# Kernel tuning notes

Hardware: AMD Instinct MI355X
Metric: run time of the kernel (lower is better)

Reference implementation:

```python
import jax, jax.numpy as jnp
import numpy as np

DIM = 1024
NUM_HEADS = 16
HEAD_DIM = DIM // NUM_HEADS


def apply_rotary_embed(x, thetas):
    # x: (..., seq, d), thetas: (seq, d) broadcast over leading dims
    x1, x2 = jnp.split(x, 2, axis=-1)
    x_rot = jnp.concatenate([-x2, x1], axis=-1)
    return x * jnp.cos(thetas) + x_rot * jnp.sin(thetas)


def setup_inputs() -> dict:
    key = jax.random.key(0)
    ks = jax.random.split(key, 8)
    B, Nx, Nc = 4, 1024, 2048
    x = jax.random.normal(ks[0], (B, Nx, DIM), dtype=jnp.float32)
    c = jax.random.normal(ks[1], (B, Nc, DIM), dtype=jnp.float32)
    x_pos_embed = jax.random.normal(ks[2], (Nx, HEAD_DIM), dtype=jnp.float32)
    c_pos_embed = jax.random.normal(ks[3], (Nc, HEAD_DIM), dtype=jnp.float32)
    s = 1.0 / np.sqrt(DIM)
    Wq = jax.random.normal(ks[4], (DIM, DIM), dtype=jnp.float32) * s
    Wkv = jax.random.normal(ks[5], (DIM, 2 * DIM), dtype=jnp.float32) * s
    Wproj = jax.random.normal(ks[6], (DIM, DIM), dtype=jnp.float32) * s
    bproj = jnp.zeros((DIM,), dtype=jnp.float32)
    return {"x": x, "c": c, "x_pos_embed": x_pos_embed, "c_pos_embed": c_pos_embed,
            "Wq": Wq, "Wkv": Wkv, "Wproj": Wproj, "bproj": bproj}


def reference(x, c, x_pos_embed, c_pos_embed, Wq, Wkv, Wproj, bproj):
    B, Nx, D = x.shape
    Nc = c.shape[1]
    H, hd = NUM_HEADS, HEAD_DIM
    # Q projection -> (B, H, Nx, hd)
    q = (x @ Wq).reshape(B, Nx, H, hd).transpose(0, 2, 1, 3)
    q = apply_rotary_embed(q, x_pos_embed)
    # KV projection -> k, v each (B, H, Nc, hd)
    kv = (c @ Wkv).reshape(B, Nc, 2, H, hd).transpose(2, 0, 3, 1, 4)
    k, v = kv[0], kv[1]
    k = apply_rotary_embed(k, c_pos_embed)
    # scaled dot-product attention (dropout p=0 -> identity)
    scale = 1.0 / np.sqrt(hd).astype(np.float32)
    attn = jnp.einsum('bhqd,bhkd->bhqk', q, k) * scale
    attn = jax.nn.softmax(attn, axis=-1)
    out = jnp.einsum('bhqk,bhkd->bhqd', attn, v)
    out = out.transpose(0, 2, 1, 3).reshape(B, Nx, D)
    return out @ Wproj + bproj
```

## Files before the change

### kernel.cpp

```cpp
#include <hip/hip_runtime.h>
#include <math.h>

#define DIMC  1024
#define NHEAD 16
#define HD    64
#define NB    4
#define NX    1024
#define NC    2048
#define KD    1024

typedef _Float16 half_t;
typedef __attribute__((ext_vector_type(8))) _Float16 h8;
typedef __attribute__((ext_vector_type(4))) _Float16 h4;
typedef __attribute__((ext_vector_type(2))) __fp16 fp16x2;
typedef __attribute__((ext_vector_type(4))) float f32x4;

#define QSCALE 0.1803368801111244f
#define NEGM  -8.656170245333781f

__device__ __forceinline__ void gload_lds16(const half_t* g, half_t* l) {
    __builtin_amdgcn_global_load_lds(
        (__attribute__((address_space(1))) void*)(g),
        (__attribute__((address_space(3))) void*)(l), 16, 0, 0);
}

__device__ __forceinline__ void wtile(const float* __restrict__ W,
                                      half_t* __restrict__ Wt, int N, int IMG,
                                      int bx, int by, int t)
{
    __shared__ half_t T[64][72];
    const int k0 = by * 64, n0 = bx * 64;
    const int kr = t >> 2, c0 = (t & 3) << 4;
    const float* src = W + (size_t)(k0 + kr) * N + n0 + c0;
#pragma unroll
    for (int j = 0; j < 16; j += 4) {
        float4 v = *(const float4*)(src + j);
        T[c0 + j + 0][kr] = (half_t)v.x;
        T[c0 + j + 1][kr] = (half_t)v.y;
        T[c0 + j + 2][kr] = (half_t)v.z;
        T[c0 + j + 3][kr] = (half_t)v.w;
    }
    __syncthreads();
    const int nr = t >> 2, kc = (t & 3) << 4;
    if (!IMG) {
        half_t* dst = Wt + (size_t)(n0 + nr) * KD + k0 + kc;
        *(int4*)dst       = *(const int4*)&T[nr][kc];
        *(int4*)(dst + 8) = *(const int4*)&T[nr][kc + 8];
    } else {
        const int n = n0 + nr;
        const int ntile = n >> 8, rr = n & 255;
        const int s0 = kc >> 3;
        half_t* base = Wt + ((size_t)(ntile * 16 + by) * 256 + rr) * 64;
        *(int4*)(base + ((s0 ^ (rr & 7)) << 3))       = *(const int4*)&T[nr][kc];
        *(int4*)(base + (((s0 + 1) ^ (rr & 7)) << 3)) = *(const int4*)&T[nr][kc + 8];
    }
}

__global__ __launch_bounds__(256) void prep(
    const float* __restrict__ x, half_t* __restrict__ xh,
    const float* __restrict__ c, half_t* __restrict__ ch,
    const float* __restrict__ xpe, const float* __restrict__ cpe,
    float* __restrict__ xct, float* __restrict__ xst,
    float* __restrict__ cct, float* __restrict__ cst,
    const float* __restrict__ Wq,  half_t* __restrict__ Wqt,
    const float* __restrict__ Wkv, half_t* __restrict__ Wkt,
    const float* __restrict__ Wp,  half_t* __restrict__ Wpt)
{
    const int bid = blockIdx.x, t = threadIdx.x;
    if (bid < 1024) {
        if (bid < 256)      wtile(Wq,  Wqt, DIMC, 0,     bid & 15,         bid >> 4,         t);
        else if (bid < 768) wtile(Wkv, Wkt, 2 * DIMC, 1, (bid - 256) & 31, (bid - 256) >> 5, t);
        else                wtile(Wp,  Wpt, DIMC, 0,     (bid - 768) & 15, (bid - 768) >> 4, t);
    } else if (bid < 7168) {
        const int nx = NB * NX * DIMC;
        const int i = ((bid - 1024) * 256 + t) * 8;
        const float* s;
        h8 o;
        if (i < nx) {
            s = x + i;
            float4 a = *(const float4*)(s);
            float4 b = *(const float4*)(s + 4);
            o[0] = (half_t)a.x; o[1] = (half_t)a.y; o[2] = (half_t)a.z; o[3] = (half_t)a.w;
            o[4] = (half_t)b.x; o[5] = (half_t)b.y; o[6] = (half_t)b.z; o[7] = (half_t)b.w;
            *(h8*)(xh + i) = o;
        } else {
            const int j = i - nx;
            s = c + j;
            float4 a = *(const float4*)(s);
            float4 b = *(const float4*)(s + 4);
            o[0] = (half_t)a.x; o[1] = (half_t)a.y; o[2] = (half_t)a.z; o[3] = (half_t)a.w;
            o[4] = (half_t)b.x; o[5] = (half_t)b.y; o[6] = (half_t)b.z; o[7] = (half_t)b.w;
            const int R = j >> 10, k = j & 1023;
            const int mt = R >> 8, r = R & 255, kt = k >> 6, sl = (k & 63) >> 3;
            *(h8*)(ch + ((size_t)(mt * 16 + kt) * 256 + r) * 64 + ((sl ^ (r & 7)) << 3)) = o;
        }
    } else {
        const int i = (bid - 7168) * 256 + t;
        if (i < NX * HD) {
            const float th = xpe[i];
            xct[i] = cosf(th); xst[i] = sinf(th);
        } else {
            const int j = i - NX * HD;
            const float th = cpe[j];
            cct[j] = cosf(th); cst[j] = sinf(th);
        }
    }
}

template <int MODE, int BN>
__global__ __launch_bounds__(256) void hgemm(
    const half_t* __restrict__ Ag, const half_t* __restrict__ Bt,
    const float* __restrict__ ct, const float* __restrict__ st,
    const float* __restrict__ bias,
    void* __restrict__ out0, void* __restrict__ out1)
{
    constexpr int MI = (BN == 128) ? 4 : 2;
    constexpr int BLOADS = BN / 32;
    __shared__ half_t As[2][8192];
    __shared__ half_t Bs[2][BN * 64];

    const int tid = threadIdx.x;
    const int w = tid >> 6, lane = tid & 63;
    const int lr = lane & 15, lg = lane >> 4;
    const int wrOff = (BN == 128) ? (w >> 1) * 64 : w * 32;
    const int wcOff = (BN == 128) ? (w & 1) * 64 : 0;

    int lin = (int)blockIdx.x;
    lin = (lin & 7) * ((int)gridDim.x >> 3) + (lin >> 3);
    const int m0 = (lin >> 4) * 128, n0 = (lin & 15) * BN;

    f32x4 acc[MI][4];
#pragma unroll
    for (int i = 0; i < MI; ++i)
#pragma unroll
        for (int j = 0; j < 4; ++j) acc[i][j] = f32x4{0.f, 0.f, 0.f, 0.f};

    size_t gA[4], gB[BLOADS];
    int loff[4];
#pragma unroll
    for (int c = 0; c < 4; ++c) {
        const int L = c * 4096 + w * 1024 + lane * 16;
        const int row = L >> 7;
        const int ss = ((L >> 4) & 7) ^ (row & 7);
        gA[c] = (size_t)(m0 + row) * KD + ss * 8;
        if (c < BLOADS) gB[c] = (size_t)(n0 + row) * KD + ss * 8;
        loff[c] = c * 2048 + w * 512;
    }

#define HSTAGE(buf, kk) do {                                               \
        _Pragma("unroll")                                                  \
        for (int c = 0; c < 4; ++c) {                                      \
            gload_lds16(Ag + gA[c] + (kk) * 64, &As[buf][loff[c]]);        \
            if (c < BLOADS) gload_lds16(Bt + gB[c] + (kk) * 64, &Bs[buf][loff[c]]); \
        }                                                                  \
    } while (0)

    HSTAGE(0, 0);
    asm volatile("s_waitcnt vmcnt(0)" ::: "memory");
    __builtin_amdgcn_s_barrier();
    __builtin_amdgcn_sched_barrier(0);

    for (int k = 0; k < KD / 64; ++k) {
        const int cb = k & 1;
        if (k + 1 < KD / 64) {
            HSTAGE(cb ^ 1, k + 1);
            if constexpr (BLOADS == 4)
                asm volatile("s_waitcnt vmcnt(8)" ::: "memory");
            else
                asm volatile("s_waitcnt vmcnt(6)" ::: "memory");
        } else {
            asm volatile("s_waitcnt vmcnt(0)" ::: "memory");
        }
        __builtin_amdgcn_s_barrier();
        __builtin_amdgcn_sched_barrier(0);

        __builtin_amdgcn_s_setprio(1);
#pragma unroll
        for (int kc = 0; kc < 2; ++kc) {
            h8 af[MI], bf[4];
#pragma unroll
            for (int mi = 0; mi < MI; ++mi) {
                const int r = wrOff + mi * 16 + lr;
                af[mi] = *(const h8*)&As[cb][r * 64 + (((kc * 4 + lg) ^ (r & 7)) << 3)];
            }
#pragma unroll
            for (int ni = 0; ni < 4; ++ni) {
                const int r = wcOff + ni * 16 + lr;
                bf[ni] = *(const h8*)&Bs[cb][r * 64 + (((kc * 4 + lg) ^ (r & 7)) << 3)];
            }
#pragma unroll
            for (int mi = 0; mi < MI; ++mi)
#pragma unroll
                for (int ni = 0; ni < 4; ++ni)
                    acc[mi][ni] = __builtin_amdgcn_mfma_f32_16x16x32_f16(
                        af[mi], bf[ni], acc[mi][ni], 0, 0, 0);
        }
        __builtin_amdgcn_s_setprio(0);

        __builtin_amdgcn_s_barrier();
        __builtin_amdgcn_sched_barrier(0);
    }
#undef HSTAGE

    if (MODE == 2) {
        float* o = (float*)out0;
#pragma unroll
        for (int ni = 0; ni < 4; ++ni) {
            const int col = n0 + ni * 16 + lr;
            const float bv = bias[col];
#pragma unroll
            for (int mi = 0; mi < MI; ++mi)
#pragma unroll
                for (int r = 0; r < 4; ++r) {
                    const int row = m0 + wrOff + mi * 16 + lg * 4 + r;
                    o[(size_t)row * DIMC + col] = acc[mi][ni][r] + bv;
                }
        }
        return;
    }

    if (MODE == 0) {
        half_t* Qw = (half_t*)out0;
        const int h = n0 >> 6;
#pragma unroll
        for (int mi = 0; mi < MI; ++mi)
#pragma unroll
            for (int r = 0; r < 4; ++r) {
                const int row = m0 + wrOff + mi * 16 + lg * 4 + r;
                const int bb = row >> 10, nn = row & (NX - 1);
                const float* cr = ct + nn * HD;
                const float* sr = st + nn * HD;
                half_t* op = Qw + (((size_t)(bb * NHEAD + h)) * NX + nn) * HD;
#pragma unroll
                for (int ni = 0; ni < 4; ++ni) {
                    const int d = ni * 16 + lr;
                    const float val = acc[mi][ni][r];
                    const float pv  = acc[mi][ni ^ 2][r];
                    op[d] = (half_t)((val * cr[d] + (ni < 2 ? -pv : pv) * sr[d]) * QSCALE);
                }
            }
    }
}

__global__ __launch_bounds__(512, 2) void hgemm_kv(
    const half_t* __restrict__ Aimg, const half_t* __restrict__ Bimg,
    const float* __restrict__ ct, const float* __restrict__ st,
    half_t* __restrict__ Kw, half_t* __restrict__ Vw)
{
    __shared__ half_t lds[65536];

    const int tid = threadIdx.x;
    const int w = tid >> 6, lane = tid & 63;
    const int lr = lane & 15, lg = lane >> 4;
    const int wr = w >> 2, wc = w & 3;
    const int wrOff = wr * 128, wcOff = wc * 64;

    int lin = (int)blockIdx.x;
    lin = (lin & 7) * 32 + (lin >> 3);
    const int mt = lin >> 3, nt = lin & 7;
    const int m0 = mt * 256, n0 = nt * 256;

    const half_t* Ablk = Aimg + (size_t)mt * 262144;
    const half_t* Bblk = Bimg + (size_t)nt * 262144;
    const int so2 = w * 512 + lane * 8;

    f32x4 acc[8][4];
#pragma unroll
    for (int i = 0; i < 8; ++i)
#pragma unroll
        for (int j = 0; j < 4; ++j) acc[i][j] = f32x4{0.f, 0.f, 0.f, 0.f};
    h8 af[2][2];
    h8 bf[4][2];

#define ISSUEH(SRC, DSTOFF) do {                                     \
        gload_lds16((SRC) + so2,        &lds[(DSTOFF) + w * 512]);   \
        gload_lds16((SRC) + 4096 + so2, &lds[(DSTOFF) + 4096 + w * 512]); \
    } while (0)

#define PHASE(MI0, AOFF, BOFF, READBF, STG, GATE) do {               \
        _Pragma("unroll")                                            \
        for (int kc = 0; kc < 2; ++kc)                               \
        _Pragma("unroll")                                            \
        for (int d = 0; d < 2; ++d) {                                \
            const int r_ = wrOff + ((MI0) + d) * 16 + lr;            \
            af[d][kc] = *(const h8*)&lds[(AOFF) + r_ * 64 + (((kc * 4 + lg) ^ (r_ & 7)) << 3)]; \
        }                                                            \
        if (READBF) {                                                \
            _Pragma("unroll")                                        \
            for (int ni = 0; ni < 4; ++ni)                           \
            _Pragma("unroll")                                        \
            for (int kc = 0; kc < 2; ++kc) {                         \
                const int rb = wcOff + ni * 16 + lr;                 \
                bf[ni][kc] = *(const h8*)&lds[(BOFF) + rb * 64 + (((kc * 4 + lg) ^ (rb & 7)) << 3)]; \
            }                                                        \
        }                                                            \
        STG;                                                         \
        __builtin_amdgcn_sched_barrier(0);                           \
        __builtin_amdgcn_s_barrier();                                \
        __builtin_amdgcn_s_setprio(1);                               \
        _Pragma("unroll")                                            \
        for (int d = 0; d < 2; ++d)                                  \
        _Pragma("unroll")                                            \
        for (int ni = 0; ni < 4; ++ni)                               \
        _Pragma("unroll")                                            \
        for (int kc = 0; kc < 2; ++kc)                               \
            acc[(MI0) + d][ni] = __builtin_amdgcn_mfma_f32_16x16x32_f16( \
                af[d][kc], bf[ni][kc], acc[(MI0) + d][ni], 0, 0, 0); \
        __builtin_amdgcn_s_setprio(0);                               \
        GATE;                                                        \
        __builtin_amdgcn_s_barrier();                                \
    } while (0)

#define GATE4 asm volatile("s_waitcnt vmcnt(4)" ::: "memory")
#define GATE0 asm volatile("s_waitcnt vmcnt(0)" ::: "memory")
#define NOG   ((void)0)

    ISSUEH(Ablk, 0);          ISSUEH(Ablk + 8192, 8192);
    ISSUEH(Bblk, 32768);      ISSUEH(Bblk + 8192, 32768 + 8192);
    __builtin_amdgcn_sched_barrier(0);
    ISSUEH(Bblk + 16384, 49152); ISSUEH(Bblk + 16384 + 8192, 49152 + 8192);
    asm volatile("s_waitcnt vmcnt(4)" ::: "memory");
    __builtin_amdgcn_s_barrier();

    for (int i = 0; i < 7; ++i) {
        const half_t* An1 = Ablk + (size_t)(2 * i + 1) * 16384;
        const half_t* An2 = Ablk + (size_t)(2 * i + 2) * 16384;
        const half_t* Bn2 = Bblk + (size_t)(2 * i + 2) * 16384;
        const half_t* Bn3 = Bblk + (size_t)(2 * i + 3) * 16384;
        PHASE(0, 0,     32768, true,  ISSUEH(An1, 16384),               NOG);
        PHASE(2, 0,     32768, false, ISSUEH(An1 + 8192, 16384 + 8192), NOG);
        PHASE(4, 0,     32768, false, ISSUEH(Bn2, 32768),               NOG);
        PHASE(6, 0,     32768, false, ISSUEH(Bn2 + 8192, 32768 + 8192), GATE4);
        PHASE(0, 16384, 49152, true,  ISSUEH(An2, 0),                   NOG);
        PHASE(2, 16384, 49152, false, ISSUEH(An2 + 8192, 8192),         NOG);
        PHASE(4, 16384, 49152, false, ISSUEH(Bn3, 49152),               NOG);
        PHASE(6, 16384, 49152, false, ISSUEH(Bn3 + 8192, 49152 + 8192), GATE4);
    }
    {
        const half_t* A15 = Ablk + (size_t)15 * 16384;
        PHASE(0, 0,     32768, true,  ISSUEH(A15, 16384),               NOG);
        PHASE(2, 0,     32768, false, ISSUEH(A15 + 8192, 16384 + 8192), NOG);
        PHASE(4, 0,     32768, false, NOG,                              NOG);
        PHASE(6, 0,     32768, false, NOG,                              GATE0);
        PHASE(0, 16384, 49152, true,  NOG,                              NOG);
        PHASE(2, 16384, 49152, false, NOG,                              NOG);
        PHASE(4, 16384, 49152, false, NOG,                              NOG);
        PHASE(6, 16384, 49152, false, NOG,                              NOG);
    }
#undef PHASE
#undef ISSUEH
#undef GATE4
#undef GATE0
#undef NOG

    const bool isK = (n0 < DIMC);
    const int h = ((n0 & (DIMC - 1)) >> 6) + wc;
#pragma unroll
    for (int mi = 0; mi < 8; ++mi)
#pragma unroll
        for (int r = 0; r < 4; ++r) {
            const int row = m0 + wrOff + mi * 16 + lg * 4 + r;
            const int bb = row >> 11, nn = row & (NC - 1);
            const int tt = nn >> 6, rr = nn & 63;
            const size_t tbase = ((size_t)(bb * NHEAD + h) * 32 + tt) * 4096;
            const float* cr = ct + nn * HD;
            const float* sr = st + nn * HD;
#pragma unroll
            for (int ni = 0; ni < 4; ++ni) {
                const int d = ni * 16 + lr;
                const float val = acc[mi][ni][r];
                if (isK) {
                    const float pv = acc[mi][ni ^ 2][r];
                    Kw[tbase + rr * 64 + ((((d >> 3) ^ (rr & 7)) << 3) | (d & 7))] =
                        (half_t)(val * cr[d] + (ni < 2 ? -pv : pv) * sr[d]);
                } else {
                    Vw[tbase + d * 64 + ((((rr >> 3) ^ (d & 7)) << 3) | (rr & 7))] =
                        (half_t)val;
                }
            }
        }
}

__global__ __launch_bounds__(256) void attn_mfma(
    const half_t* __restrict__ Q, const half_t* __restrict__ Kg,
    const half_t* __restrict__ Vg, half_t* __restrict__ O)
{
    __shared__ half_t Ks[2][4096];
    __shared__ half_t Vs[2][4096];
    __shared__ half_t Ps[8192];

    const int tid = threadIdx.x;
    const int w = tid >> 6, lane = tid & 63;
    const int lr = lane & 15, lg = lane >> 4;
    const int e7 = lr & 7;

    const int sid = (blockIdx.x & 7) * 64 + (blockIdx.x >> 3);
    const int bh = sid >> 3;
    const int q0 = (sid & 7) * 128;
    const int b = bh >> 4, h = bh & 15;

    const half_t* qbase = Q + ((size_t)bh * NX + q0 + w * 16 + lr) * HD + lg * 8;
    const h8 qf0a = *(const h8*)(qbase);
    const h8 qf1a = *(const h8*)(qbase + 32);
    const h8 qf0b = *(const h8*)(qbase + (size_t)64 * HD);
    const h8 qf1b = *(const h8*)(qbase + (size_t)64 * HD + 32);

    f32x4 acc[2][4];
#pragma unroll
    for (int qb = 0; qb < 2; ++qb)
#pragma unroll
        for (int i = 0; i < 4; ++i) acc[qb][i] = f32x4{0.f, 0.f, 0.f, 0.f};
    f32x4 accl[2] = {{0.f, 0.f, 0.f, 0.f}, {0.f, 0.f, 0.f, 0.f}};

    h8 vone;
#pragma unroll
    for (int i = 0; i < 8; ++i) vone[i] = (half_t)(lr == 0 ? 1.0f : 0.0f);

    const half_t* Kt = Kg + (size_t)bh * 32 * 4096;
    const half_t* Vt = Vg + (size_t)bh * 32 * 4096;
    const int so = w * 512 + lane * 8;

#define STAGE(bi, t) do {                                           \
        const half_t* kg_ = Kt + (size_t)(t) * 4096;                \
        const half_t* vg_ = Vt + (size_t)(t) * 4096;                \
        gload_lds16(kg_ + so,        &Ks[bi][w * 512]);             \
        gload_lds16(kg_ + 2048 + so, &Ks[bi][2048 + w * 512]);      \
        gload_lds16(vg_ + so,        &Vs[bi][w * 512]);             \
        gload_lds16(vg_ + 2048 + so, &Vs[bi][2048 + w * 512]);      \
    } while (0)

    STAGE(0, 0);
    asm volatile("s_waitcnt vmcnt(0)" ::: "memory");
    __builtin_amdgcn_s_barrier();
    __builtin_amdgcn_sched_barrier(0);

    const int rowq = w * 16 + lr;

    for (int t = 0; t < NC / 64; ++t) {
        const int cur = t & 1;
        if (t + 1 < NC / 64) {
            STAGE(cur ^ 1, t + 1);
            asm volatile("s_waitcnt vmcnt(8)" ::: "memory");
        } else {
            asm volatile("s_waitcnt vmcnt(0)" ::: "memory");
        }
        __builtin_amdgcn_s_barrier();
        __builtin_amdgcn_sched_barrier(0);

        h8 kfr[4][2];
#pragma unroll
        for (int cb = 0; cb < 4; ++cb) {
            const int r = cb * 16 + lr;
            kfr[cb][0] = *(const h8*)&Ks[cur][r * 64 + ((lg ^ e7) << 3)];
            kfr[cb][1] = *(const h8*)&Ks[cur][r * 64 + (((4 + lg) ^ e7) << 3)];
        }

#pragma unroll
        for (int qb = 0; qb < 2; ++qb) {
            const h8 q0f = qb ? qf0b : qf0a;
            const h8 q1f = qb ? qf1b : qf1a;
            const int rowp = qb * 64 + rowq;

            f32x4 sc[4];
            __builtin_amdgcn_s_setprio(1);
#pragma unroll
            for (int cb = 0; cb < 4; ++cb) {
                f32x4 a = {NEGM, NEGM, NEGM, NEGM};
                a = __builtin_amdgcn_mfma_f32_16x16x32_f16(kfr[cb][0], q0f, a, 0, 0, 0);
                a = __builtin_amdgcn_mfma_f32_16x16x32_f16(kfr[cb][1], q1f, a, 0, 0, 0);
                sc[cb] = a;
            }
            __builtin_amdgcn_s_setprio(0);

#pragma unroll
            for (int cb = 0; cb < 4; ++cb) {
                fp16x2 a01 = __builtin_amdgcn_cvt_pkrtz(exp2f(sc[cb][0]), exp2f(sc[cb][1]));
                fp16x2 a23 = __builtin_amdgcn_cvt_pkrtz(exp2f(sc[cb][2]), exp2f(sc[cb][3]));
                union { h4 h; uint2 u; } pw;
                pw.u.x = *(unsigned int*)&a01;
                pw.u.y = *(unsigned int*)&a23;
                const int s = cb * 2 + (lg >> 1);
                *(h4*)&Ps[rowp * 64 + ((s ^ e7) << 3) + (lg & 1) * 4] = pw.h;
            }
        }

        h8 pf[2][2];
#pragma unroll
        for (int qb = 0; qb < 2; ++qb) {
            const int rowp = qb * 64 + rowq;
            pf[qb][0] = *(const h8*)&Ps[rowp * 64 + ((lg ^ e7) << 3)];
            pf[qb][1] = *(const h8*)&Ps[rowp * 64 + (((4 + lg) ^ e7) << 3)];
        }

        __builtin_amdgcn_s_setprio(1);
#pragma unroll
        for (int db = 0; db < 4; ++db) {
            const int rd = db * 16 + lr;
            const h8 vf0 = *(const h8*)&Vs[cur][rd * 64 + ((lg ^ e7) << 3)];
            const h8 vf1 = *(const h8*)&Vs[cur][rd * 64 + (((4 + lg) ^ e7) << 3)];
#pragma unroll
            for (int qb = 0; qb < 2; ++qb) {
                acc[qb][db] = __builtin_amdgcn_mfma_f32_16x16x32_f16(pf[qb][0], vf0, acc[qb][db], 0, 0, 0);
                acc[qb][db] = __builtin_amdgcn_mfma_f32_16x16x32_f16(pf[qb][1], vf1, acc[qb][db], 0, 0, 0);
            }
        }
#pragma unroll
        for (int qb = 0; qb < 2; ++qb) {
            accl[qb] = __builtin_amdgcn_mfma_f32_16x16x32_f16(pf[qb][0], vone, accl[qb], 0, 0, 0);
            accl[qb] = __builtin_amdgcn_mfma_f32_16x16x32_f16(pf[qb][1], vone, accl[qb], 0, 0, 0);
        }
        __builtin_amdgcn_s_setprio(0);

        __builtin_amdgcn_s_barrier();
        __builtin_amdgcn_sched_barrier(0);
    }
#undef STAGE

    half_t* Ob = O + ((size_t)b * NX + q0 + w * 16) * DIMC + h * HD;
#pragma unroll
    for (int qb = 0; qb < 2; ++qb) {
        float invs[4];
#pragma unroll
        for (int r = 0; r < 4; ++r)
            invs[r] = 1.f / __shfl(accl[qb][r], lg << 4);
#pragma unroll
        for (int db = 0; db < 4; ++db)
#pragma unroll
            for (int r = 0; r < 4; ++r)
                Ob[(size_t)(qb * 64 + lg * 4 + r) * DIMC + db * 16 + lr] =
                    (half_t)(acc[qb][db][r] * invs[r]);
    }
}

extern "C" void kernel_launch(void* const* d_in, const int* in_sizes, int n_in,
                              void* d_out, int out_size, void* d_ws, size_t ws_size,
                              hipStream_t stream)
{
    const float* x     = (const float*)d_in[0];
    const float* c     = (const float*)d_in[1];
    const float* xpe   = (const float*)d_in[2];
    const float* cpe   = (const float*)d_in[3];
    const float* Wq    = (const float*)d_in[4];
    const float* Wkv   = (const float*)d_in[5];
    const float* Wproj = (const float*)d_in[6];
    const float* bproj = (const float*)d_in[7];

    char* wsb = (char*)d_ws;
    half_t* xh  = (half_t*)(wsb);
    half_t* ch  = (half_t*)(wsb + ((size_t)8  << 20));
    half_t* Wqt = (half_t*)(wsb + ((size_t)24 << 20));
    half_t* Wkt = (half_t*)(wsb + ((size_t)26 << 20));
    half_t* Wpt = (half_t*)(wsb + ((size_t)30 << 20));
    half_t* Kw  = (half_t*)(wsb + ((size_t)32 << 20));
    half_t* Vw  = (half_t*)(wsb + ((size_t)48 << 20));
    half_t* Ow  = (half_t*)(wsb + ((size_t)64 << 20));
    float*  xct = (float*)(wsb + ((size_t)72 << 20));
    float*  xst = (float*)(wsb + ((size_t)72 << 20) + (256u << 10));
    float*  cct = (float*)(wsb + ((size_t)72 << 20) + (512u << 10));
    float*  cst = (float*)(wsb + ((size_t)72 << 20) + (1024u << 10));
    half_t* Qw  = (half_t*)d_out;

    prep<<<7936, 256, 0, stream>>>(x, xh, c, ch, xpe, cpe,
                                   xct, xst, cct, cst,
                                   Wq, Wqt, Wkv, Wkt, Wproj, Wpt);

    hgemm<0, 64><<<512, 256, 0, stream>>>(xh, Wqt, xct, xst, nullptr,
                                          Qw, nullptr);
    hgemm_kv<<<256, 512, 0, stream>>>(ch, Wkt, cct, cst, Kw, Vw);
    attn_mfma<<<512, 256, 0, stream>>>(Qw, Kw, Vw, Ow);
    hgemm<2, 64><<<512, 256, 0, stream>>>(Ow, Wpt, nullptr, nullptr, bproj,
                                          (float*)d_out, nullptr);
}
```

Before: 183.3 us.

## Split attention over two KV halves and add a combine kernel

Each attention block now processes only half of the key/value tiles, doubling the grid from 512 to 1024 blocks. Each block writes unnormalized fp32 partial outputs and row sums to workspace. A new combine kernel adds the two halves, normalizes, and writes the fp16 output for the projection GEMM. This aims to raise parallelism and latency hiding on the many-CU device. In exchange it adds fp32 partial-buffer traffic, an extra kernel launch, and moves the Wpt workspace location.

```diff
diff --git a/kernel.cpp b/kernel.cpp
--- a/kernel.cpp
+++ b/kernel.cpp
@@ -383,7 +383,8 @@
 
 __global__ __launch_bounds__(256) void attn_mfma(
     const half_t* __restrict__ Q, const half_t* __restrict__ Kg,
-    const half_t* __restrict__ Vg, half_t* __restrict__ O)
+    const half_t* __restrict__ Vg,
+    float* __restrict__ Opart, float* __restrict__ Lpart)
 {
     __shared__ half_t Ks[2][4096];
     __shared__ half_t Vs[2][4096];
@@ -394,10 +395,11 @@
     const int lr = lane & 15, lg = lane >> 4;
     const int e7 = lr & 7;
 
-    const int sid = (blockIdx.x & 7) * 64 + (blockIdx.x >> 3);
+    const int inner = (int)blockIdx.x & 511;
+    const int kvh = (int)blockIdx.x >> 9;
+    const int sid = (inner & 7) * 64 + (inner >> 3);
     const int bh = sid >> 3;
     const int q0 = (sid & 7) * 128;
-    const int b = bh >> 4, h = bh & 15;
 
     const half_t* qbase = Q + ((size_t)bh * NX + q0 + w * 16 + lr) * HD + lg * 8;
     const h8 qf0a = *(const h8*)(qbase);
@@ -419,6 +421,7 @@
     const half_t* Kt = Kg + (size_t)bh * 32 * 4096;
     const half_t* Vt = Vg + (size_t)bh * 32 * 4096;
     const int so = w * 512 + lane * 8;
+    const int t0 = kvh * 16, t1 = t0 + 16;
 
 #define STAGE(bi, t) do {                                           \
         const half_t* kg_ = Kt + (size_t)(t) * 4096;                \
@@ -429,18 +432,18 @@
         gload_lds16(vg_ + 2048 + so, &Vs[bi][2048 + w * 512]);      \
     } while (0)
 
-    STAGE(0, 0);
+    STAGE(0, t0);
     asm volatile("s_waitcnt vmcnt(0)" ::: "memory");
     __builtin_amdgcn_s_barrier();
     __builtin_amdgcn_sched_barrier(0);
 
     const int rowq = w * 16 + lr;
 
-    for (int t = 0; t < NC / 64; ++t) {
+    for (int t = t0; t < t1; ++t) {
         const int cur = t & 1;
-        if (t + 1 < NC / 64) {
+        if (t + 1 < t1) {
             STAGE(cur ^ 1, t + 1);
-            asm volatile("s_waitcnt vmcnt(8)" ::: "memory");
+            asm volatile("s_waitcnt vmcnt(4)" ::: "memory");
         } else {
             asm volatile("s_waitcnt vmcnt(0)" ::: "memory");
         }
@@ -516,19 +519,57 @@
     }
 #undef STAGE
 
-    half_t* Ob = O + ((size_t)b * NX + q0 + w * 16) * DIMC + h * HD;
 #pragma unroll
     for (int qb = 0; qb < 2; ++qb) {
-        float invs[4];
-#pragma unroll
-        for (int r = 0; r < 4; ++r)
-            invs[r] = 1.f / __shfl(accl[qb][r], lg << 4);
+        const int qblk = (q0 >> 6) + qb;
+        const int slot = (bh * 16 + qblk) * 2 + kvh;
+        float* Po = Opart + (size_t)slot * 4096;
 #pragma unroll
         for (int db = 0; db < 4; ++db)
 #pragma unroll
             for (int r = 0; r < 4; ++r)
-                Ob[(size_t)(qb * 64 + lg * 4 + r) * DIMC + db * 16 + lr] =
-                    (half_t)(acc[qb][db][r] * invs[r]);
+                Po[(w * 16 + lg * 4 + r) * 64 + db * 16 + lr] = acc[qb][db][r];
+        if (lr == 0) {
+#pragma unroll
+            for (int r = 0; r < 4; ++r)
+                Lpart[(size_t)slot * 64 + w * 16 + lg * 4 + r] = accl[qb][r];
+        }
+    }
+}
+
+__global__ __launch_bounds__(256) void combine(
+    const float* __restrict__ Opart, const float* __restrict__ Lpart,
+    half_t* __restrict__ Ow)
+{
+    const int pidx = blockIdx.x;
+    const int bh = pidx >> 4, qblk = pidx & 15;
+    const int b = bh >> 4, h = bh & 15;
+    const int t = threadIdx.x;
+    const int row = t >> 2;
+    const int c0 = (t & 3) << 4;
+
+    const float* P0 = Opart + (size_t)(pidx * 2 + 0) * 4096 + row * 64 + c0;
+    const float* P1 = Opart + (size_t)(pidx * 2 + 1) * 4096 + row * 64 + c0;
+    const float inv = 1.f / (Lpart[(size_t)(pidx * 2 + 0) * 64 + row] +
+                             Lpart[(size_t)(pidx * 2 + 1) * 64 + row]);
+
+    half_t* o = Ow + ((size_t)b * NX + qblk * 64 + row) * DIMC + h * 64 + c0;
+#pragma unroll
+    for (int j = 0; j < 16; j += 8) {
+        float4 a0 = *(const float4*)(P0 + j);
+        float4 a1 = *(const float4*)(P0 + j + 4);
+        float4 b0 = *(const float4*)(P1 + j);
+        float4 b1 = *(const float4*)(P1 + j + 4);
+        h8 ov;
+        ov[0] = (half_t)((a0.x + b0.x) * inv);
+        ov[1] = (half_t)((a0.y + b0.y) * inv);
+        ov[2] = (half_t)((a0.z + b0.z) * inv);
+        ov[3] = (half_t)((a0.w + b0.w) * inv);
+        ov[4] = (half_t)((a1.x + b1.x) * inv);
+        ov[5] = (half_t)((a1.y + b1.y) * inv);
+        ov[6] = (half_t)((a1.z + b1.z) * inv);
+        ov[7] = (half_t)((a1.w + b1.w) * inv);
+        *(h8*)(o + j) = ov;
     }
 }
 
@@ -550,7 +591,6 @@
     half_t* ch  = (half_t*)(wsb + ((size_t)8  << 20));
     half_t* Wqt = (half_t*)(wsb + ((size_t)24 << 20));
     half_t* Wkt = (half_t*)(wsb + ((size_t)26 << 20));
-    half_t* Wpt = (half_t*)(wsb + ((size_t)30 << 20));
     half_t* Kw  = (half_t*)(wsb + ((size_t)32 << 20));
     half_t* Vw  = (half_t*)(wsb + ((size_t)48 << 20));
     half_t* Ow  = (half_t*)(wsb + ((size_t)64 << 20));
@@ -558,6 +598,9 @@
     float*  xst = (float*)(wsb + ((size_t)72 << 20) + (256u << 10));
     float*  cct = (float*)(wsb + ((size_t)72 << 20) + (512u << 10));
     float*  cst = (float*)(wsb + ((size_t)72 << 20) + (1024u << 10));
+    half_t* Wpt = (half_t*)(wsb + ((size_t)74 << 20));
+    float*  Lpart = (float*)(wsb + ((size_t)76 << 20));
+    float*  Opart = (float*)(wsb);
     half_t* Qw  = (half_t*)d_out;
 
     prep<<<7936, 256, 0, stream>>>(x, xh, c, ch, xpe, cpe,
@@ -567,7 +610,8 @@
     hgemm<0, 64><<<512, 256, 0, stream>>>(xh, Wqt, xct, xst, nullptr,
                                           Qw, nullptr);
     hgemm_kv<<<256, 512, 0, stream>>>(ch, Wkt, cct, cst, Kw, Vw);
-    attn_mfma<<<512, 256, 0, stream>>>(Qw, Kw, Vw, Ow);
+    attn_mfma<<<1024, 256, 0, stream>>>(Qw, Kw, Vw, Opart, Lpart);
+    combine<<<1024, 256, 0, stream>>>(Opart, Lpart, Ow);
     hgemm<2, 64><<<512, 256, 0, stream>>>(Ow, Wpt, nullptr, nullptr, bproj,
                                           (float*)d_out, nullptr);
 }
```

Measured after the change: 184.3 us (median of 2 runs). No clear change (+0.5%).
